# Performance work log

Hardware: AMD Instinct MI355X
Metric: run time of the kernel (lower is better)

Reference implementation:

```python
import jax, jax.numpy as jnp
import numpy as np

D_MODEL = 1024
N_HEADS = 16
HEAD_DIM = D_MODEL // N_HEADS
BATCH = 4
SEQ = 2048


def setup_inputs() -> dict:
    key = jax.random.key(0)
    ks = jax.random.split(key, 5)
    # Xavier uniform bound for square d_model x d_model weights
    bound = np.sqrt(6.0 / (D_MODEL + D_MODEL))
    x = jax.random.normal(ks[0], (BATCH, SEQ, D_MODEL), dtype=jnp.float32)
    attention_mask = jnp.ones((BATCH, SEQ), dtype=jnp.int32)
    wq = jax.random.uniform(ks[1], (D_MODEL, D_MODEL), jnp.float32, -bound, bound)
    wk = jax.random.uniform(ks[2], (D_MODEL, D_MODEL), jnp.float32, -bound, bound)
    wv = jax.random.uniform(ks[3], (D_MODEL, D_MODEL), jnp.float32, -bound, bound)
    wo = jax.random.uniform(ks[4], (D_MODEL, D_MODEL), jnp.float32, -bound, bound)
    return {"x": x, "attention_mask": attention_mask,
            "wq": wq, "wk": wk, "wv": wv, "wo": wo}


def reference(x, attention_mask, wq, wk, wv, wo):
    # x: (B, S, D). Linear weights stored torch-style (out, in): y = x @ W^T
    B, S, D = x.shape
    H, Hd = N_HEADS, HEAD_DIM
    scale = np.sqrt(Hd).astype(np.float32)

    def split_heads(t):  # (B,S,D) -> (B,H,S,Hd)
        return t.reshape(B, S, H, Hd).transpose(0, 2, 1, 3)

    q = split_heads(jnp.einsum('bsd,ed->bse', x, wq))
    k = split_heads(jnp.einsum('bsd,ed->bse', x, wk))
    v = split_heads(jnp.einsum('bsd,ed->bse', x, wv))

    scores = jnp.einsum('bhqd,bhkd->bhqk', q, k) / scale  # (B,H,S,S)

    causal = jnp.tril(jnp.ones((S, S), dtype=bool))  # True = keep
    keep = causal[None, None, :, :] & (attention_mask[:, None, None, :] != 0)
    scores = jnp.where(keep, scores, -jnp.inf)

    attn = jax.nn.softmax(scores, axis=-1)  # dropout: eval mode (identity)
    out = jnp.einsum('bhqk,bhkd->bhqd', attn, v)  # (B,H,S,Hd)
    out = out.transpose(0, 2, 1, 3).reshape(B, S, D)
    return jnp.einsum('bsd,ed->bse', out, wo)
```

## Files before the change

### kernel.cpp

```cpp
#include <hip/hip_runtime.h>
#include <cstdint>
#include <cstddef>

#define D_MODEL 1024
#define N_HEADS 16
#define HEAD_DIM 64
#define BATCH 4
#define SEQ 2048
#define M_TOTAL (BATCH * SEQ)

typedef __attribute__((ext_vector_type(8))) short bf16x8;
typedef __attribute__((ext_vector_type(4))) float f32x4;
typedef __attribute__((ext_vector_type(16))) float f32x16;

#define Q_SCALE 0.18033688011112042f

__device__ __forceinline__ unsigned short f2bu(float f) {
    union { float f; unsigned u; } x; x.f = f;
    unsigned r = x.u + 0x7FFFu + ((x.u >> 16) & 1u);
    return (unsigned short)(r >> 16);
}

__device__ __forceinline__ void async16(void* lds, const void* g) {
    __builtin_amdgcn_global_load_lds(
        (const __attribute__((address_space(1))) void*)g,
        (__attribute__((address_space(3))) void*)lds, 16, 0, 0);
}

__global__ __launch_bounds__(256) void cast_all(const float* __restrict__ x,
                                                const float* __restrict__ wq,
                                                const float* __restrict__ wk,
                                                const float* __restrict__ wv,
                                                const float* __restrict__ wo,
                                                unsigned short* __restrict__ dst) {
    const size_t NE = (size_t)M_TOTAL * D_MODEL;
    const size_t WE = (size_t)D_MODEL * D_MODEL;
    size_t i4 = (size_t)blockIdx.x * 256 + threadIdx.x;
    size_t e = i4 * 4;
    const float* src; size_t off;
    if (e < NE) { src = x; off = e; }
    else {
        size_t t = e - NE;
        int r = (int)(t / WE); off = t - (size_t)r * WE;
        src = (r == 0) ? wq : (r == 1) ? wk : (r == 2) ? wv : wo;
    }
    float4 v = *(const float4*)(src + off);
    ushort4 o;
    o.x = f2bu(v.x); o.y = f2bu(v.y); o.z = f2bu(v.z); o.w = f2bu(v.w);
    ((ushort4*)dst)[i4] = o;
}

__global__ __launch_bounds__(256) void qkv_gemm(const unsigned short* __restrict__ X,
                                                const unsigned short* __restrict__ W0,
                                                const unsigned short* __restrict__ W1,
                                                const unsigned short* __restrict__ W2,
                                                unsigned short* __restrict__ Y0,
                                                unsigned short* __restrict__ Y1,
                                                unsigned short* __restrict__ Y2) {
    __shared__ short As[128 * 32];
    __shared__ short Bs[128 * 32];

    const int sel = blockIdx.x >> 3;
    const unsigned short* W = (sel == 0) ? W0 : (sel == 1) ? W1 : W2;
    unsigned short* Y = (sel == 0) ? Y0 : (sel == 1) ? Y1 : Y2;
    const float scl = (sel == 0) ? Q_SCALE : 1.0f;

    const int tid = threadIdx.x;
    const int w = tid >> 6, lane = tid & 63, quad = lane >> 4, l15 = lane & 15;
    const int wm = w & 1, wn = w >> 1;
    const int rowBase = blockIdx.y * 128;
    const int colBase = (blockIdx.x & 7) * 128;

    f32x4 acc[4][4];
#pragma unroll
    for (int mi = 0; mi < 4; ++mi)
#pragma unroll
        for (int ni = 0; ni < 4; ++ni)
#pragma unroll
            for (int e = 0; e < 4; ++e) acc[mi][ni][e] = 0.f;

    for (int k0 = 0; k0 < 1024; k0 += 32) {
        __syncthreads();
#pragma unroll
        for (int l = 0; l < 2; ++l) {
            int c = tid + l * 256;
            int row = c >> 2, ccs = c & 3;
            int cc = ccs ^ ((row >> 1) & 3);
            async16((char*)As + c * 16, X + (size_t)(rowBase + row) * 1024 + k0 + cc * 8);
            async16((char*)Bs + c * 16, W + (size_t)(colBase + row) * 1024 + k0 + cc * 8);
        }
        __syncthreads();

        bf16x8 a[4], b[4];
#pragma unroll
        for (int mi = 0; mi < 4; ++mi) {
            int r = wm * 64 + mi * 16 + l15;
            int slot = quad ^ ((r >> 1) & 3);
            a[mi] = *(const bf16x8*)&As[r * 32 + slot * 8];
        }
#pragma unroll
        for (int ni = 0; ni < 4; ++ni) {
            int r = wn * 64 + ni * 16 + l15;
            int slot = quad ^ ((r >> 1) & 3);
            b[ni] = *(const bf16x8*)&Bs[r * 32 + slot * 8];
        }
#pragma unroll
        for (int mi = 0; mi < 4; ++mi)
#pragma unroll
            for (int ni = 0; ni < 4; ++ni)
                acc[mi][ni] = __builtin_amdgcn_mfma_f32_16x16x32_bf16(a[mi], b[ni], acc[mi][ni], 0, 0, 0);
    }

#pragma unroll
    for (int mi = 0; mi < 4; ++mi)
#pragma unroll
        for (int ni = 0; ni < 4; ++ni)
#pragma unroll
            for (int reg = 0; reg < 4; ++reg) {
                int row = rowBase + wm * 64 + mi * 16 + quad * 4 + reg;
                int col = colBase + wn * 64 + ni * 16 + l15;
                Y[(size_t)row * 1024 + col] = f2bu(acc[mi][ni][reg] * scl);
            }
}

__global__ __launch_bounds__(256) void out_gemm(const unsigned short* __restrict__ X,
                                                const unsigned short* __restrict__ W,
                                                float* __restrict__ Y) {
    __shared__ short As[128 * 32];
    __shared__ short Bs[128 * 32];

    const int tid = threadIdx.x;
    const int w = tid >> 6, lane = tid & 63, quad = lane >> 4, l15 = lane & 15;
    const int wm = w & 1, wn = w >> 1;
    const int rowBase = blockIdx.y * 128;
    const int colBase = blockIdx.x * 128;

    f32x4 acc[4][4];
#pragma unroll
    for (int mi = 0; mi < 4; ++mi)
#pragma unroll
        for (int ni = 0; ni < 4; ++ni)
#pragma unroll
            for (int e = 0; e < 4; ++e) acc[mi][ni][e] = 0.f;

    for (int k0 = 0; k0 < 1024; k0 += 32) {
        __syncthreads();
#pragma unroll
        for (int l = 0; l < 2; ++l) {
            int c = tid + l * 256;
            int row = c >> 2, ccs = c & 3;
            int cc = ccs ^ ((row >> 1) & 3);
            async16((char*)As + c * 16, X + (size_t)(rowBase + row) * 1024 + k0 + cc * 8);
            async16((char*)Bs + c * 16, W + (size_t)(colBase + row) * 1024 + k0 + cc * 8);
        }
        __syncthreads();

        bf16x8 a[4], b[4];
#pragma unroll
        for (int mi = 0; mi < 4; ++mi) {
            int r = wm * 64 + mi * 16 + l15;
            int slot = quad ^ ((r >> 1) & 3);
            a[mi] = *(const bf16x8*)&As[r * 32 + slot * 8];
        }
#pragma unroll
        for (int ni = 0; ni < 4; ++ni) {
            int r = wn * 64 + ni * 16 + l15;
            int slot = quad ^ ((r >> 1) & 3);
            b[ni] = *(const bf16x8*)&Bs[r * 32 + slot * 8];
        }
#pragma unroll
        for (int mi = 0; mi < 4; ++mi)
#pragma unroll
            for (int ni = 0; ni < 4; ++ni)
                acc[mi][ni] = __builtin_amdgcn_mfma_f32_16x16x32_bf16(a[mi], b[ni], acc[mi][ni], 0, 0, 0);
    }

#pragma unroll
    for (int mi = 0; mi < 4; ++mi)
#pragma unroll
        for (int ni = 0; ni < 4; ++ni)
#pragma unroll
            for (int reg = 0; reg < 4; ++reg) {
                int row = rowBase + wm * 64 + mi * 16 + quad * 4 + reg;
                int col = colBase + wn * 64 + ni * 16 + l15;
                Y[(size_t)row * 1024 + col] = acc[mi][ni][reg];
            }
}

__global__ __launch_bounds__(256) void transpose_v(const unsigned short* __restrict__ V,
                                                   unsigned short* __restrict__ Vt) {
    const int st = blockIdx.x;
    const int bh = blockIdx.y;
    const int b = bh >> 4, h = bh & 15;
    const int tid = threadIdx.x;
    const int s0 = st * 64;
    __shared__ unsigned short Ts[64 * 72];

#pragma unroll
    for (int l = 0; l < 2; ++l) {
        int c = tid + l * 256;
        int s = c >> 3, cc = c & 7;
        *(uint4*)&Ts[s * 72 + cc * 8] =
            *(const uint4*)&V[(size_t)(b * SEQ + s0 + s) * D_MODEL + h * HEAD_DIM + cc * 8];
    }
    __syncthreads();
#pragma unroll
    for (int l = 0; l < 2; ++l) {
        int c = tid + l * 256;
        int d = c >> 3, sc = c & 7;
        unsigned short tmp[8];
#pragma unroll
        for (int j = 0; j < 8; ++j) tmp[j] = Ts[(sc * 8 + j) * 72 + d];
        *(uint4*)&Vt[((size_t)bh * HEAD_DIM + d) * SEQ + s0 + sc * 8] = *(uint4*)tmp;
    }
}

__global__ __launch_bounds__(256) void flash32(const unsigned short* __restrict__ Q,
                                               const unsigned short* __restrict__ K,
                                               const unsigned short* __restrict__ Vt,
                                               const int* __restrict__ mask,
                                               unsigned short* __restrict__ CTX) {
    __shared__ short lds[9216];
    __shared__ float biasS[64];
    __shared__ int allokS;

    short* Ks = lds;
    short* Vs = lds + 4096;

    const int qt = 15 - (int)blockIdx.x;
    const int bh = blockIdx.y;
    const int b = bh >> 4, h = bh & 15;
    const int tid = threadIdx.x;
    const int w = tid >> 6, lane = tid & 63, l31 = lane & 31, lane5 = lane >> 5;
    const int q0 = qt * 128;

    const size_t qkBase = (size_t)b * SEQ * D_MODEL + (size_t)h * HEAD_DIM;
    const size_t vtBase = (size_t)bh * HEAD_DIM * SEQ;

    const int iq = q0 + w * 32 + l31;
    bf16x8 qf[4];
#pragma unroll
    for (int ks = 0; ks < 4; ++ks)
        qf[ks] = *(const bf16x8*)(Q + qkBase + (size_t)iq * D_MODEL + ks * 16 + lane5 * 8);

    float mv = -INFINITY, lv = 0.f;
    f32x16 Ot[2];
#pragma unroll
    for (int dt = 0; dt < 2; ++dt)
#pragma unroll
        for (int e = 0; e < 16; ++e) Ot[dt][e] = 0.f;

    const int ktmax = 2 * qt + 1;
    for (int kt = 0; kt <= ktmax; ++kt) {
        const int k0 = kt * 64;
        __syncthreads();
#pragma unroll
        for (int l = 0; l < 2; ++l) {
            int c = tid + l * 256;
            int p = c >> 3, sl = c & 7;
            int cc = sl ^ (p & 7);
            int j = (p & 0x33) | ((p & 4) << 1) | ((p & 8) >> 1);
            async16((char*)Ks + c * 16, K + qkBase + (size_t)(k0 + j) * D_MODEL + cc * 8);
            async16((char*)Vs + c * 16, Vt + vtBase + (size_t)p * SEQ + k0 + cc * 8);
        }
        if (tid < 64) {
            int mk = mask[b * SEQ + k0 + tid];
            biasS[tid] = mk ? 0.f : -INFINITY;
            unsigned long long bal = __ballot(mk != 0);
            if (tid == 0) allokS = (bal == ~0ull) ? 1 : 0;
        }
        __syncthreads();

        if (64 * kt > q0 + 32 * w + 31) continue;

        f32x16 St[2];
#pragma unroll
        for (int T = 0; T < 2; ++T)
#pragma unroll
            for (int e = 0; e < 16; ++e) St[T][e] = 0.f;
#pragma unroll
        for (int T = 0; T < 2; ++T)
#pragma unroll
            for (int ks = 0; ks < 4; ++ks) {
                int p = T * 32 + l31;
                int slot = (ks * 2 + lane5) ^ (p & 7);
                bf16x8 a = *(const bf16x8*)&Ks[p * 64 + slot * 8];
                St[T] = __builtin_amdgcn_mfma_f32_32x32x16_bf16(a, qf[ks], St[T], 0, 0, 0);
            }

        const bool partial = (k0 + 63 > q0 + 32 * w);
        if (partial) {
#pragma unroll
            for (int T = 0; T < 2; ++T)
#pragma unroll
                for (int r = 0; r < 16; ++r) {
                    int j = k0 + 32 * T + 16 * (r >> 3) + 8 * lane5 + (r & 7);
                    if (j > iq) St[T][r] = -INFINITY;
                }
        }
        if (!allokS) {
#pragma unroll
            for (int T = 0; T < 2; ++T)
#pragma unroll
                for (int r = 0; r < 16; ++r)
                    St[T][r] += biasS[32 * T + 16 * (r >> 3) + 8 * lane5 + (r & 7)];
        }

        float rm = -INFINITY;
#pragma unroll
        for (int T = 0; T < 2; ++T)
#pragma unroll
            for (int r = 0; r < 16; ++r) rm = fmaxf(rm, St[T][r]);
        rm = fmaxf(rm, __shfl_xor(rm, 32));
        float mn = fmaxf(mv, rm);
        float al = (mv > -INFINITY) ? exp2f(mv - mn) : 0.f;
        float rs = 0.f;
#pragma unroll
        for (int T = 0; T < 2; ++T)
#pragma unroll
            for (int r = 0; r < 16; ++r) {
                float pv = (St[T][r] > -INFINITY) ? exp2f(St[T][r] - mn) : 0.f;
                St[T][r] = pv;
                rs += pv;
            }
        rs += __shfl_xor(rs, 32);
        lv = lv * al + rs;
        mv = mn;
#pragma unroll
        for (int dt = 0; dt < 2; ++dt)
#pragma unroll
            for (int e = 0; e < 16; ++e) Ot[dt][e] *= al;

        bf16x8 pf[4];
#pragma unroll
        for (int t = 0; t < 4; ++t) {
            int T = t >> 1, hb = t & 1;
#pragma unroll
            for (int jj = 0; jj < 8; ++jj)
                pf[t][jj] = (short)f2bu(St[T][hb * 8 + jj]);
        }

#pragma unroll
        for (int dt = 0; dt < 2; ++dt)
#pragma unroll
            for (int t = 0; t < 4; ++t) {
                int p = dt * 32 + l31;
                int slot = (t * 2 + lane5) ^ (p & 7);
                bf16x8 a = *(const bf16x8*)&Vs[p * 64 + slot * 8];
                Ot[dt] = __builtin_amdgcn_mfma_f32_32x32x16_bf16(a, pf[t], Ot[dt], 0, 0, 0);
            }
    }

    __syncthreads();
    const float inv = 1.f / lv;
#pragma unroll
    for (int dt = 0; dt < 2; ++dt)
#pragma unroll
        for (int k = 0; k < 8; ++k) {
            int r0 = 2 * k;
            int d = (r0 & 3) + 4 * lane5 + 8 * (r0 >> 2) + 32 * dt;
            unsigned lo = f2bu(Ot[dt][r0] * inv);
            unsigned hi = f2bu(Ot[dt][r0 + 1] * inv);
            *(unsigned*)&lds[(w * 32 + l31) * 72 + d] = lo | (hi << 16);
        }
    __syncthreads();
#pragma unroll
    for (int k = 0; k < 4; ++k) {
        int id = tid + k * 256;
        int r = id >> 3, cc = id & 7;
        uint4 v = *(const uint4*)&lds[r * 72 + cc * 8];
        *(uint4*)(CTX + qkBase + (size_t)(q0 + r) * D_MODEL + cc * 8) = v;
    }
}

extern "C" void kernel_launch(void* const* d_in, const int* in_sizes, int n_in,
                              void* d_out, int out_size, void* d_ws, size_t ws_size,
                              hipStream_t stream) {
    const float* x  = (const float*)d_in[0];
    const int* mask = (const int*)d_in[1];
    const float* wq = (const float*)d_in[2];
    const float* wk = (const float*)d_in[3];
    const float* wv = (const float*)d_in[4];
    const float* wo = (const float*)d_in[5];
    float* out = (float*)d_out;

    const size_t NE = (size_t)M_TOTAL * D_MODEL;
    const size_t WE = (size_t)D_MODEL * D_MODEL;
    unsigned short* ws  = (unsigned short*)d_ws;
    unsigned short* xb  = ws;
    unsigned short* wqb = xb + NE;
    unsigned short* wkb = wqb + WE;
    unsigned short* wvb = wkb + WE;
    unsigned short* wob = wvb + WE;
    unsigned short* Qb  = wob + WE;
    unsigned short* Kb  = Qb + NE;
    unsigned short* Vb  = Kb + NE;
    unsigned short* Vtb = Vb + NE;
    unsigned short* CTX = Vb;

    cast_all<<<(int)((NE + 4 * WE) / 4 / 256), 256, 0, stream>>>(x, wq, wk, wv, wo, ws);

    qkv_gemm<<<dim3(24, M_TOTAL / 128), 256, 0, stream>>>(xb, wqb, wkb, wvb, Qb, Kb, Vb);

    transpose_v<<<dim3(SEQ / 64, BATCH * N_HEADS), 256, 0, stream>>>(Vb, Vtb);

    flash32<<<dim3(SEQ / 128, BATCH * N_HEADS), 256, 0, stream>>>(Qb, Kb, Vtb, mask, CTX);

    out_gemm<<<dim3(D_MODEL / 128, M_TOTAL / 128), 256, 0, stream>>>(CTX, wob, out);
}
```

Before: 362.3 us.

## Fuse V transpose into QKV GEMM, pair causal tiles, register-prefetch K/V

The QKV GEMM now writes V directly in the head-transposed layout, so the separate transpose kernel and its extra memory round trip are gone. The flash kernel launches half as many blocks, and each block handles a long and a short query tile (15-p and p) to balance causal work. Async global-to-LDS loads are replaced by register prefetch of the next K/V tile, overlapping loads with compute. P is converted to bf16 with a cheaper rounding. Risks: fewer blocks (512) may underfill the GPU, the transposed stores from the GEMM are narrow, and register pressure rises.

```diff
diff --git a/kernel.cpp b/kernel.cpp
--- a/kernel.cpp
+++ b/kernel.cpp
@@ -19,6 +19,10 @@
     union { float f; unsigned u; } x; x.f = f;
     unsigned r = x.u + 0x7FFFu + ((x.u >> 16) & 1u);
     return (unsigned short)(r >> 16);
+}
+__device__ __forceinline__ unsigned short f2bu_fast(float f) {
+    union { float f; unsigned u; } x; x.f = f;
+    return (unsigned short)((x.u + 0x8000u) >> 16);
 }
 
 __device__ __forceinline__ void async16(void* lds, const void* g) {
@@ -56,13 +60,12 @@
                                                 const unsigned short* __restrict__ W2,
                                                 unsigned short* __restrict__ Y0,
                                                 unsigned short* __restrict__ Y1,
-                                                unsigned short* __restrict__ Y2) {
+                                                unsigned short* __restrict__ Vt) {
     __shared__ short As[128 * 32];
     __shared__ short Bs[128 * 32];
 
     const int sel = blockIdx.x >> 3;
     const unsigned short* W = (sel == 0) ? W0 : (sel == 1) ? W1 : W2;
-    unsigned short* Y = (sel == 0) ? Y0 : (sel == 1) ? Y1 : Y2;
     const float scl = (sel == 0) ? Q_SCALE : 1.0f;
 
     const int tid = threadIdx.x;
@@ -111,16 +114,35 @@
                 acc[mi][ni] = __builtin_amdgcn_mfma_f32_16x16x32_bf16(a[mi], b[ni], acc[mi][ni], 0, 0, 0);
     }
 
-#pragma unroll
-    for (int mi = 0; mi < 4; ++mi)
-#pragma unroll
-        for (int ni = 0; ni < 4; ++ni)
-#pragma unroll
-            for (int reg = 0; reg < 4; ++reg) {
-                int row = rowBase + wm * 64 + mi * 16 + quad * 4 + reg;
+    if (sel != 2) {
+        unsigned short* Y = (sel == 0) ? Y0 : Y1;
+#pragma unroll
+        for (int mi = 0; mi < 4; ++mi)
+#pragma unroll
+            for (int ni = 0; ni < 4; ++ni)
+#pragma unroll
+                for (int reg = 0; reg < 4; ++reg) {
+                    int row = rowBase + wm * 64 + mi * 16 + quad * 4 + reg;
+                    int col = colBase + wn * 64 + ni * 16 + l15;
+                    Y[(size_t)row * 1024 + col] = f2bu(acc[mi][ni][reg] * scl);
+                }
+    } else {
+#pragma unroll
+        for (int mi = 0; mi < 4; ++mi) {
+            int row0 = rowBase + wm * 64 + mi * 16 + quad * 4;
+            int bb = row0 >> 11;
+            int s0 = row0 & 2047;
+#pragma unroll
+            for (int ni = 0; ni < 4; ++ni) {
                 int col = colBase + wn * 64 + ni * 16 + l15;
-                Y[(size_t)row * 1024 + col] = f2bu(acc[mi][ni][reg] * scl);
-            }
+                int hh = col >> 6, dd = col & 63;
+                ushort4 pk;
+                pk.x = f2bu(acc[mi][ni][0]); pk.y = f2bu(acc[mi][ni][1]);
+                pk.z = f2bu(acc[mi][ni][2]); pk.w = f2bu(acc[mi][ni][3]);
+                *(ushort4*)(Vt + (((size_t)bb * 16 + hh) * 64 + dd) * SEQ + s0) = pk;
+            }
+        }
+    }
 }
 
 __global__ __launch_bounds__(256) void out_gemm(const unsigned short* __restrict__ X,
@@ -185,34 +207,6 @@
                 int col = colBase + wn * 64 + ni * 16 + l15;
                 Y[(size_t)row * 1024 + col] = acc[mi][ni][reg];
             }
-}
-
-__global__ __launch_bounds__(256) void transpose_v(const unsigned short* __restrict__ V,
-                                                   unsigned short* __restrict__ Vt) {
-    const int st = blockIdx.x;
-    const int bh = blockIdx.y;
-    const int b = bh >> 4, h = bh & 15;
-    const int tid = threadIdx.x;
-    const int s0 = st * 64;
-    __shared__ unsigned short Ts[64 * 72];
-
-#pragma unroll
-    for (int l = 0; l < 2; ++l) {
-        int c = tid + l * 256;
-        int s = c >> 3, cc = c & 7;
-        *(uint4*)&Ts[s * 72 + cc * 8] =
-            *(const uint4*)&V[(size_t)(b * SEQ + s0 + s) * D_MODEL + h * HEAD_DIM + cc * 8];
-    }
-    __syncthreads();
-#pragma unroll
-    for (int l = 0; l < 2; ++l) {
-        int c = tid + l * 256;
-        int d = c >> 3, sc = c & 7;
-        unsigned short tmp[8];
-#pragma unroll
-        for (int j = 0; j < 8; ++j) tmp[j] = Ts[(sc * 8 + j) * 72 + d];
-        *(uint4*)&Vt[((size_t)bh * HEAD_DIM + d) * SEQ + s0 + sc * 8] = *(uint4*)tmp;
-    }
 }
 
 __global__ __launch_bounds__(256) void flash32(const unsigned short* __restrict__ Q,
@@ -227,149 +221,181 @@
     short* Ks = lds;
     short* Vs = lds + 4096;
 
-    const int qt = 15 - (int)blockIdx.x;
+    const int pid = blockIdx.x;
     const int bh = blockIdx.y;
-    const int b = bh >> 4, h = bh & 15;
+    const int b = bh >> 4;
     const int tid = threadIdx.x;
     const int w = tid >> 6, lane = tid & 63, l31 = lane & 31, lane5 = lane >> 5;
-    const int q0 = qt * 128;
-
-    const size_t qkBase = (size_t)b * SEQ * D_MODEL + (size_t)h * HEAD_DIM;
+
+    const size_t qkBase = (size_t)b * SEQ * D_MODEL + (size_t)(bh & 15) * HEAD_DIM;
     const size_t vtBase = (size_t)bh * HEAD_DIM * SEQ;
 
-    const int iq = q0 + w * 32 + l31;
-    bf16x8 qf[4];
-#pragma unroll
-    for (int ks = 0; ks < 4; ++ks)
-        qf[ks] = *(const bf16x8*)(Q + qkBase + (size_t)iq * D_MODEL + ks * 16 + lane5 * 8);
-
-    float mv = -INFINITY, lv = 0.f;
-    f32x16 Ot[2];
-#pragma unroll
-    for (int dt = 0; dt < 2; ++dt)
-#pragma unroll
-        for (int e = 0; e < 16; ++e) Ot[dt][e] = 0.f;
-
-    const int ktmax = 2 * qt + 1;
-    for (int kt = 0; kt <= ktmax; ++kt) {
-        const int k0 = kt * 64;
-        __syncthreads();
-#pragma unroll
-        for (int l = 0; l < 2; ++l) {
-            int c = tid + l * 256;
-            int p = c >> 3, sl = c & 7;
-            int cc = sl ^ (p & 7);
-            int j = (p & 0x33) | ((p & 4) << 1) | ((p & 8) >> 1);
-            async16((char*)Ks + c * 16, K + qkBase + (size_t)(k0 + j) * D_MODEL + cc * 8);
-            async16((char*)Vs + c * 16, Vt + vtBase + (size_t)p * SEQ + k0 + cc * 8);
-        }
-        if (tid < 64) {
-            int mk = mask[b * SEQ + k0 + tid];
-            biasS[tid] = mk ? 0.f : -INFINITY;
-            unsigned long long bal = __ballot(mk != 0);
-            if (tid == 0) allokS = (bal == ~0ull) ? 1 : 0;
-        }
-        __syncthreads();
-
-        if (64 * kt > q0 + 32 * w + 31) continue;
-
-        f32x16 St[2];
-#pragma unroll
-        for (int T = 0; T < 2; ++T)
-#pragma unroll
-            for (int e = 0; e < 16; ++e) St[T][e] = 0.f;
-#pragma unroll
-        for (int T = 0; T < 2; ++T)
-#pragma unroll
-            for (int ks = 0; ks < 4; ++ks) {
-                int p = T * 32 + l31;
-                int slot = (ks * 2 + lane5) ^ (p & 7);
-                bf16x8 a = *(const bf16x8*)&Ks[p * 64 + slot * 8];
-                St[T] = __builtin_amdgcn_mfma_f32_32x32x16_bf16(a, qf[ks], St[T], 0, 0, 0);
-            }
-
-        const bool partial = (k0 + 63 > q0 + 32 * w);
-        if (partial) {
+    int stp[2], stcc[2], stj[2];
+#pragma unroll
+    for (int l = 0; l < 2; ++l) {
+        int c = tid + l * 256;
+        int p = c >> 3, sl = c & 7;
+        stp[l] = p;
+        stcc[l] = sl ^ (p & 7);
+        stj[l] = (p & 0x33) | ((p & 4) << 1) | ((p & 8) >> 1);
+    }
+
+    for (int phase = 0; phase < 2; ++phase) {
+        const int qt = phase ? pid : 15 - pid;
+        const int q0 = qt * 128;
+        const int iq = q0 + w * 32 + l31;
+
+        bf16x8 qf[4];
+#pragma unroll
+        for (int ks = 0; ks < 4; ++ks)
+            qf[ks] = *(const bf16x8*)(Q + qkBase + (size_t)iq * D_MODEL + ks * 16 + lane5 * 8);
+
+        float mv = -INFINITY, lv = 0.f;
+        f32x16 Ot[2];
+#pragma unroll
+        for (int dt = 0; dt < 2; ++dt)
+#pragma unroll
+            for (int e = 0; e < 16; ++e) Ot[dt][e] = 0.f;
+
+        const int ktmax = 2 * qt + 1;
+
+        uint4 kreg[2], vreg[2];
+        int mreg;
+        {
+            const int k0 = 0;
+#pragma unroll
+            for (int l = 0; l < 2; ++l) {
+                kreg[l] = *(const uint4*)(K + qkBase + (size_t)(k0 + stj[l]) * D_MODEL + stcc[l] * 8);
+                vreg[l] = *(const uint4*)(Vt + vtBase + (size_t)stp[l] * SEQ + k0 + stcc[l] * 8);
+            }
+            mreg = (tid < 64) ? mask[b * SEQ + k0 + tid] : 1;
+        }
+
+        for (int kt = 0; kt <= ktmax; ++kt) {
+            const int k0 = kt * 64;
+            __syncthreads();
+#pragma unroll
+            for (int l = 0; l < 2; ++l) {
+                int c = tid + l * 256;
+                *(uint4*)((char*)Ks + c * 16) = kreg[l];
+                *(uint4*)((char*)Vs + c * 16) = vreg[l];
+            }
+            if (tid < 64) {
+                biasS[tid] = mreg ? 0.f : -INFINITY;
+                unsigned long long bal = __ballot(mreg != 0);
+                if (tid == 0) allokS = (bal == ~0ull) ? 1 : 0;
+            }
+            if (kt < ktmax) {
+                const int kn = k0 + 64;
+#pragma unroll
+                for (int l = 0; l < 2; ++l) {
+                    kreg[l] = *(const uint4*)(K + qkBase + (size_t)(kn + stj[l]) * D_MODEL + stcc[l] * 8);
+                    vreg[l] = *(const uint4*)(Vt + vtBase + (size_t)stp[l] * SEQ + kn + stcc[l] * 8);
+                }
+                mreg = (tid < 64) ? mask[b * SEQ + kn + tid] : 1;
+            }
+            __syncthreads();
+
+            if (64 * kt > q0 + 32 * w + 31) continue;
+
+            f32x16 St[2];
 #pragma unroll
             for (int T = 0; T < 2; ++T)
 #pragma unroll
+                for (int e = 0; e < 16; ++e) St[T][e] = 0.f;
+#pragma unroll
+            for (int T = 0; T < 2; ++T)
+#pragma unroll
+                for (int ks = 0; ks < 4; ++ks) {
+                    int p = T * 32 + l31;
+                    int slot = (ks * 2 + lane5) ^ (p & 7);
+                    bf16x8 a = *(const bf16x8*)&Ks[p * 64 + slot * 8];
+                    St[T] = __builtin_amdgcn_mfma_f32_32x32x16_bf16(a, qf[ks], St[T], 0, 0, 0);
+                }
+
+            const bool partial = (k0 + 63 > q0 + 32 * w);
+            if (partial) {
+#pragma unroll
+                for (int T = 0; T < 2; ++T)
+#pragma unroll
+                    for (int r = 0; r < 16; ++r) {
+                        int j = k0 + 32 * T + 16 * (r >> 3) + 8 * lane5 + (r & 7);
+                        if (j > iq) St[T][r] = -INFINITY;
+                    }
+            }
+            if (!allokS) {
+#pragma unroll
+                for (int T = 0; T < 2; ++T)
+#pragma unroll
+                    for (int r = 0; r < 16; ++r)
+                        St[T][r] += biasS[32 * T + 16 * (r >> 3) + 8 * lane5 + (r & 7)];
+            }
+
+            float rm = -INFINITY;
+#pragma unroll
+            for (int T = 0; T < 2; ++T)
+#pragma unroll
+                for (int r = 0; r < 16; ++r) rm = fmaxf(rm, St[T][r]);
+            rm = fmaxf(rm, __shfl_xor(rm, 32));
+            float mn = fmaxf(mv, rm);
+            float al = (mv > -INFINITY) ? exp2f(mv - mn) : 0.f;
+            float rs = 0.f;
+#pragma unroll
+            for (int T = 0; T < 2; ++T)
+#pragma unroll
                 for (int r = 0; r < 16; ++r) {
-                    int j = k0 + 32 * T + 16 * (r >> 3) + 8 * lane5 + (r & 7);
-                    if (j > iq) St[T][r] = -INFINITY;
+                    float pv = (St[T][r] > -INFINITY) ? exp2f(St[T][r] - mn) : 0.f;
+                    St[T][r] = pv;
+                    rs += pv;
                 }
-        }
-        if (!allokS) {
-#pragma unroll
-            for (int T = 0; T < 2; ++T)
-#pragma unroll
-                for (int r = 0; r < 16; ++r)
-                    St[T][r] += biasS[32 * T + 16 * (r >> 3) + 8 * lane5 + (r & 7)];
-        }
-
-        float rm = -INFINITY;
-#pragma unroll
-        for (int T = 0; T < 2; ++T)
-#pragma unroll
-            for (int r = 0; r < 16; ++r) rm = fmaxf(rm, St[T][r]);
-        rm = fmaxf(rm, __shfl_xor(rm, 32));
-        float mn = fmaxf(mv, rm);
-        float al = (mv > -INFINITY) ? exp2f(mv - mn) : 0.f;
-        float rs = 0.f;
-#pragma unroll
-        for (int T = 0; T < 2; ++T)
-#pragma unroll
-            for (int r = 0; r < 16; ++r) {
-                float pv = (St[T][r] > -INFINITY) ? exp2f(St[T][r] - mn) : 0.f;
-                St[T][r] = pv;
-                rs += pv;
-            }
-        rs += __shfl_xor(rs, 32);
-        lv = lv * al + rs;
-        mv = mn;
+            rs += __shfl_xor(rs, 32);
+            lv = lv * al + rs;
+            mv = mn;
+#pragma unroll
+            for (int dt = 0; dt < 2; ++dt)
+#pragma unroll
+                for (int e = 0; e < 16; ++e) Ot[dt][e] *= al;
+
+            bf16x8 pf[4];
+#pragma unroll
+            for (int t = 0; t < 4; ++t) {
+                int T = t >> 1, hb = t & 1;
+#pragma unroll
+                for (int jj = 0; jj < 8; ++jj)
+                    pf[t][jj] = (short)f2bu_fast(St[T][hb * 8 + jj]);
+            }
+
+#pragma unroll
+            for (int dt = 0; dt < 2; ++dt)
+#pragma unroll
+                for (int t = 0; t < 4; ++t) {
+                    int p = dt * 32 + l31;
+                    int slot = (t * 2 + lane5) ^ (p & 7);
+                    bf16x8 a = *(const bf16x8*)&Vs[p * 64 + slot * 8];
+                    Ot[dt] = __builtin_amdgcn_mfma_f32_32x32x16_bf16(a, pf[t], Ot[dt], 0, 0, 0);
+                }
+        }
+
+        __syncthreads();
+        const float inv = 1.f / lv;
 #pragma unroll
         for (int dt = 0; dt < 2; ++dt)
 #pragma unroll
-            for (int e = 0; e < 16; ++e) Ot[dt][e] *= al;
-
-        bf16x8 pf[4];
-#pragma unroll
-        for (int t = 0; t < 4; ++t) {
-            int T = t >> 1, hb = t & 1;
-#pragma unroll
-            for (int jj = 0; jj < 8; ++jj)
-                pf[t][jj] = (short)f2bu(St[T][hb * 8 + jj]);
-        }
-
-#pragma unroll
-        for (int dt = 0; dt < 2; ++dt)
-#pragma unroll
-            for (int t = 0; t < 4; ++t) {
-                int p = dt * 32 + l31;
-                int slot = (t * 2 + lane5) ^ (p & 7);
-                bf16x8 a = *(const bf16x8*)&Vs[p * 64 + slot * 8];
-                Ot[dt] = __builtin_amdgcn_mfma_f32_32x32x16_bf16(a, pf[t], Ot[dt], 0, 0, 0);
-            }
-    }
-
-    __syncthreads();
-    const float inv = 1.f / lv;
-#pragma unroll
-    for (int dt = 0; dt < 2; ++dt)
-#pragma unroll
-        for (int k = 0; k < 8; ++k) {
-            int r0 = 2 * k;
-            int d = (r0 & 3) + 4 * lane5 + 8 * (r0 >> 2) + 32 * dt;
-            unsigned lo = f2bu(Ot[dt][r0] * inv);
-            unsigned hi = f2bu(Ot[dt][r0 + 1] * inv);
-            *(unsigned*)&lds[(w * 32 + l31) * 72 + d] = lo | (hi << 16);
-        }
-    __syncthreads();
-#pragma unroll
-    for (int k = 0; k < 4; ++k) {
-        int id = tid + k * 256;
-        int r = id >> 3, cc = id & 7;
-        uint4 v = *(const uint4*)&lds[r * 72 + cc * 8];
-        *(uint4*)(CTX + qkBase + (size_t)(q0 + r) * D_MODEL + cc * 8) = v;
+            for (int k = 0; k < 8; ++k) {
+                int r0 = 2 * k;
+                int d = (r0 & 3) + 4 * lane5 + 8 * (r0 >> 2) + 32 * dt;
+                unsigned lo = f2bu(Ot[dt][r0] * inv);
+                unsigned hi = f2bu(Ot[dt][r0 + 1] * inv);
+                *(unsigned*)&lds[(w * 32 + l31) * 72 + d] = lo | (hi << 16);
+            }
+        __syncthreads();
+#pragma unroll
+        for (int k = 0; k < 4; ++k) {
+            int id = tid + k * 256;
+            int r = id >> 3, cc = id & 7;
+            uint4 v = *(const uint4*)&lds[r * 72 + cc * 8];
+            *(uint4*)(CTX + qkBase + (size_t)(q0 + r) * D_MODEL + cc * 8) = v;
+        }
     }
 }
 
@@ -394,17 +420,14 @@
     unsigned short* wob = wvb + WE;
     unsigned short* Qb  = wob + WE;
     unsigned short* Kb  = Qb + NE;
-    unsigned short* Vb  = Kb + NE;
-    unsigned short* Vtb = Vb + NE;
-    unsigned short* CTX = Vb;
+    unsigned short* Vtb = Kb + NE;
+    unsigned short* CTX = Vtb + NE;
 
     cast_all<<<(int)((NE + 4 * WE) / 4 / 256), 256, 0, stream>>>(x, wq, wk, wv, wo, ws);
 
-    qkv_gemm<<<dim3(24, M_TOTAL / 128), 256, 0, stream>>>(xb, wqb, wkb, wvb, Qb, Kb, Vb);
-
-    transpose_v<<<dim3(SEQ / 64, BATCH * N_HEADS), 256, 0, stream>>>(Vb, Vtb);
-
-    flash32<<<dim3(SEQ / 128, BATCH * N_HEADS), 256, 0, stream>>>(Qb, Kb, Vtb, mask, CTX);
+    qkv_gemm<<<dim3(24, M_TOTAL / 128), 256, 0, stream>>>(xb, wqb, wkb, wvb, Qb, Kb, Vtb);
+
+    flash32<<<dim3(8, BATCH * N_HEADS), 256, 0, stream>>>(Qb, Kb, Vtb, mask, CTX);
 
     out_gemm<<<dim3(D_MODEL / 128, M_TOTAL / 128), 256, 0, stream>>>(CTX, wob, out);
 }
```

After: 316.1 us. 1.15x faster.
